# Kernel optimization log

Hardware: AMD Instinct MI355X
Metric: run time of the kernel (lower is better)

## Reference

```python
import jax, jax.numpy as jnp
import numpy as np

NUM_NODES = 4
WEIGHT = 2
IN_C = 128
OUT_C = 128
N = 128
T = 512
BN_EPS = 1e-5


def _shift_index(A, node_num, channels, weight):
    """Faithful numpy port of Modified_shift_gcn.shift(). A: binarized [V,V]."""
    idx = np.arange(node_num * channels).reshape(node_num, channels)
    idx_copy = idx.copy()
    for i in range(node_num):
        current_A = A[i].copy()
        current_A[i] = 0
        neighbors = np.nonzero(current_A)[0]
        j = 0
        counter_i = i + 1
        while j < channels:
            next_node = counter_i % node_num
            if j < weight:
                j += weight
            elif next_node == i:
                j += weight
                counter_i += 1
            elif next_node in neighbors:
                idx[i][j:j + weight] = idx_copy[next_node][j:j + weight]
                j += weight
                counter_i += 1
            else:
                idx[i][j] = idx_copy[next_node][j]
                j += 1
                counter_i += 1
    return idx.flatten()


def setup_inputs() -> dict:
    key = jax.random.key(0)
    k1, k2 = jax.random.split(key)
    # A summed over num_subset then binarized, as in __init__
    adj = np.array([[0, 1, 0, 1], [1, 0, 1, 0], [0, 1, 0, 1], [1, 0, 1, 0]], dtype=np.float64)
    A = np.stack([adj, adj, adj]).sum(0)
    A = (A != 0).astype(np.float64)
    shift_in = jnp.asarray(_shift_index(A.copy(), NUM_NODES, IN_C, WEIGHT), dtype=jnp.int32)
    shift_out = jnp.asarray(_shift_index(A.copy(), NUM_NODES, OUT_C, WEIGHT), dtype=jnp.int32)
    x = jax.random.normal(k1, (N, IN_C, T, NUM_NODES), dtype=jnp.float32)
    Linear_weight = jax.random.normal(k2, (IN_C, OUT_C), dtype=jnp.float32) * float(np.sqrt(1.0 / OUT_C))
    Linear_bias = jnp.zeros((1, 1, OUT_C), dtype=jnp.float32)
    Feature_Mask = jnp.zeros((1, NUM_NODES, IN_C), dtype=jnp.float32)
    bn_gamma = jnp.ones((NUM_NODES * OUT_C,), dtype=jnp.float32)
    bn_beta = jnp.zeros((NUM_NODES * OUT_C,), dtype=jnp.float32)
    return {"x": x, "Linear_weight": Linear_weight, "Linear_bias": Linear_bias,
            "Feature_Mask": Feature_Mask, "bn_gamma": bn_gamma, "bn_beta": bn_beta,
            "shift_in": shift_in, "shift_out": shift_out}


def reference(x, Linear_weight, Linear_bias, Feature_Mask, bn_gamma, bn_beta, shift_in, shift_out):
    n, c, t, v = x.shape
    d = Linear_weight.shape[1]
    # [N,C,T,V] -> [N*T, V*C]
    h = jnp.transpose(x, (0, 2, 3, 1)).reshape(n * t, v * c)
    # shift-in gather
    h = jnp.take(h, shift_in, axis=1)
    # feature mask (tanh + 1) and pointwise linear over channels
    h = h.reshape(n * t, v, c) * (jnp.tanh(Feature_Mask) + 1.0)
    h = jnp.einsum('nvc,cd->nvd', h, Linear_weight) + Linear_bias
    # shift-out gather
    h = h.reshape(n * t, v * d)
    h = jnp.take(h, shift_out, axis=1)
    # BatchNorm1d over the N*T batch dim (training-mode batch stats, biased var)
    mean = jnp.mean(h, axis=0)
    var = jnp.mean(jnp.square(h - mean), axis=0)
    h = (h - mean) * jax.lax.rsqrt(var + BN_EPS) * bn_gamma + bn_beta
    # back to [N,C_out,T,V], residual (down is identity since in==out), ReLU
    out = jnp.transpose(h.reshape(n, t, v, d), (0, 3, 1, 2))
    return jax.nn.relu(out + x)
```

## Files before the change

### kernel.cpp

```cpp
#include <hip/hip_runtime.h>

typedef __attribute__((ext_vector_type(4))) float f32x4;
typedef __attribute__((ext_vector_type(8))) short s16x8;

#define DEV __device__ __forceinline__

namespace {
constexpr int CH = 128;
constexpr int TDIM = 512;
constexpr int NBLK = 512;
constexpr float INV_ROWS = 1.0f / 65536.0f;
constexpr float EPS = 1e-5f;

DEV unsigned short f2bf(float f) {
  unsigned int u = __float_as_uint(f);
  u = (u + 0x7FFFu + ((u >> 16) & 1u)) >> 16;
  return (unsigned short)u;
}

DEV unsigned int pack2bf(float lo, float hi) {
  unsigned int ua = __float_as_uint(lo) + 0x8000u;
  unsigned int ub = __float_as_uint(hi) + 0x8000u;
#if __has_builtin(__builtin_amdgcn_perm)
  return __builtin_amdgcn_perm(ub, ua, 0x07060302u);
#else
  return (ub & 0xFFFF0000u) | (ua >> 16);
#endif
}

DEV void lds_barrier() {
  asm volatile("s_waitcnt lgkmcnt(0)" ::: "memory");
  __builtin_amdgcn_s_barrier();
  asm volatile("" ::: "memory");
}

DEV float maskval(float x) { return 2.0f / (1.0f + __expf(-2.0f * x)); }

DEV int xgi(int b, int v, int t, int c) {
  return (((b << 2) + v) * 16 + t) * 128 + (c ^ ((t & 7) << 3));
}
}

template <int PHASE>
__global__ __launch_bounds__(512) void gcn_fused(
    const float* __restrict__ x, const float* __restrict__ W,
    const float* __restrict__ FM, const int* __restrict__ shin,
    const int* __restrict__ shout, const float* __restrict__ tab,
    float* __restrict__ part, float* __restrict__ out) {
  __shared__ __align__(16) unsigned short xg[2 * 4 * 16 * 128];

  const int tid = threadIdx.x;
  const int lane = tid & 63;
  const int w = tid >> 6;
  const int g4 = lane >> 4;
  const int l16 = lane & 15;
  const int dbase = w * 16;

  const int bid = blockIdx.x;
  const int n = bid >> 2;
  const int tb = (bid & 3) * 128;

  const int tlow = tid & 7;
  const int c0 = (tid >> 3) * 2;

  float mk[2][4];
  unsigned int svp = 0;
#pragma unroll
  for (int i = 0; i < 2; ++i)
#pragma unroll
    for (int v = 0; v < 4; ++v) {
      int j = v * CH + (c0 + i);
      mk[i][v] = maskval(FM[j]);
      svp |= (unsigned int)((shin[j] >> 7) & 3) << ((i * 4 + v) * 2);
    }

  s16x8 wt[4];
#pragma unroll
  for (int kk = 0; kk < 4; ++kk) {
    s16x8 f;
#pragma unroll
    for (int e = 0; e < 8; ++e)
      f[e] = (short)f2bf(W[(kk * 32 + g4 * 8 + e) * CH + dbase + l16]);
    wt[kk] = f;
  }

  unsigned int svo = 0;
  if (PHASE == 2) {
#pragma unroll
    for (int r = 0; r < 4; ++r) {
      int d = dbase + g4 * 4 + r;
#pragma unroll
      for (int v = 0; v < 4; ++v)
        svo |= (unsigned int)((shout[v * CH + d] >> 7) & 3) << (r * 8 + v * 2);
    }
  }

  float s2[4][4];
  f32x4 rs[2];
  if (PHASE == 1) {
#pragma unroll
    for (int vo = 0; vo < 4; ++vo)
#pragma unroll
      for (int r = 0; r < 4; ++r) s2[vo][r] = 0.f;
    rs[0] = f32x4{0.f, 0.f, 0.f, 0.f};
    rs[1] = f32x4{0.f, 0.f, 0.f, 0.f};
  }

  const f32x4* xf4 = (const f32x4*)x;
  const float2* tab2 = (const float2*)tab;

  f32x4 pa[2][2], pb[2][2];
  f32x4 res[2][4];

#define LOADT(SLOT, TILE)                                                 \
  {                                                                       \
    _Pragma("unroll") for (int h = 0; h < 2; ++h) {                       \
      const int tgl = tb + (TILE) * 16 + h * 8 + tlow;                    \
      pa[SLOT][h] = xf4[(n * CH + c0) * TDIM + tgl];                      \
      pb[SLOT][h] = xf4[(n * CH + c0 + 1) * TDIM + tgl];                  \
    }                                                                     \
  }

#define RESLOAD(SLOT, TILE)                                               \
  {                                                                       \
    const int tgr = tb + (TILE) * 16 + l16;                               \
    _Pragma("unroll") for (int r = 0; r < 4; ++r) res[SLOT][r] =          \
        xf4[(n * CH + dbase + g4 * 4 + r) * TDIM + tgr];                  \
  }

#define STAGE(BUF, SLOT)                                                  \
  {                                                                       \
    _Pragma("unroll") for (int h = 0; h < 2; ++h) {                       \
      const int t = h * 8 + tlow;                                         \
      if (PHASE == 1) {                                                   \
        rs[0] += pa[SLOT][h];                                             \
        rs[1] += pb[SLOT][h];                                             \
      }                                                                   \
      _Pragma("unroll") for (int v = 0; v < 4; ++v) {                     \
        int s0 = (svp >> ((0 * 4 + v) * 2)) & 3;                          \
        float a = pa[SLOT][h][0];                                         \
        a = (s0 == 1) ? pa[SLOT][h][1] : a;                               \
        a = (s0 == 2) ? pa[SLOT][h][2] : a;                               \
        a = (s0 == 3) ? pa[SLOT][h][3] : a;                               \
        a *= mk[0][v];                                                    \
        int s1 = (svp >> ((1 * 4 + v) * 2)) & 3;                          \
        float b = pb[SLOT][h][0];                                         \
        b = (s1 == 1) ? pb[SLOT][h][1] : b;                               \
        b = (s1 == 2) ? pb[SLOT][h][2] : b;                               \
        b = (s1 == 3) ? pb[SLOT][h][3] : b;                               \
        b *= mk[1][v];                                                    \
        *(unsigned int*)&xg[xgi(BUF, v, t, c0)] = pack2bf(a, b);          \
      }                                                                   \
    }                                                                     \
  }

  {
    LOADT(0, 0)
    LOADT(1, 1)
    if (PHASE == 2) RESLOAD(0, 0)
    STAGE(0, 0)
  }

#pragma unroll
  for (int tile = 0; tile < 8; ++tile) {
    const int buf = tile & 1;
    lds_barrier();

    if (tile < 6) LOADT(buf, tile + 2)
    if (PHASE == 2 && tile < 7) RESLOAD(buf ^ 1, tile + 1)

    f32x4 acc[4];
    const f32x4 z4 = {0.f, 0.f, 0.f, 0.f};
#pragma unroll
    for (int vo = 0; vo < 4; ++vo) acc[vo] = z4;
#pragma unroll
    for (int vo = 0; vo < 4; ++vo) {
      s16x8 bfr[4];
#pragma unroll
      for (int kk = 0; kk < 4; ++kk)
        bfr[kk] = *(const s16x8*)&xg[xgi(buf, vo, l16, kk * 32 + g4 * 8)];
#pragma unroll
      for (int kk = 0; kk < 4; ++kk)
        acc[vo] = __builtin_amdgcn_mfma_f32_16x16x32_bf16(wt[kk], bfr[kk], acc[vo], 0, 0, 0);
    }

    if (PHASE == 1) {
#pragma unroll
      for (int vo = 0; vo < 4; ++vo)
#pragma unroll
        for (int r = 0; r < 4; ++r) s2[vo][r] = fmaf(acc[vo][r], acc[vo][r], s2[vo][r]);
    } else {
      const int tg = tb + tile * 16 + l16;
#pragma unroll
      for (int r = 0; r < 4; ++r) {
        const int d = dbase + g4 * 4 + r;
        f32x4 o;
#pragma unroll
        for (int v = 0; v < 4; ++v) {
          int sv = (svo >> (r * 8 + v * 2)) & 3;
          float ov = acc[0][r];
          ov = (sv == 1) ? acc[1][r] : ov;
          ov = (sv == 2) ? acc[2][r] : ov;
          ov = (sv == 3) ? acc[3][r] : ov;
          float2 ssv = tab2[v * CH + d];
          float y = fmaf(ov, ssv.x, ssv.y) + res[buf][r][v];
          o[v] = fmaxf(y, 0.f);
        }
        *(f32x4*)&out[((n * CH + d) * TDIM + tg) * 4] = o;
      }
    }

    if (tile < 7) STAGE(buf ^ 1, buf ^ 1)
  }
#undef STAGE
#undef RESLOAD
#undef LOADT

  if (PHASE == 1) {
#pragma unroll
    for (int vo = 0; vo < 4; ++vo)
#pragma unroll
      for (int r = 0; r < 4; ++r) {
        float v = s2[vo][r];
        v += __shfl_xor(v, 1, 64);
        v += __shfl_xor(v, 2, 64);
        v += __shfl_xor(v, 4, 64);
        v += __shfl_xor(v, 8, 64);
        if (l16 == 0) part[(vo * CH + dbase + g4 * 4 + r) * NBLK + bid] = v;
      }
#pragma unroll
    for (int i = 0; i < 2; ++i)
#pragma unroll
      for (int v = 0; v < 4; ++v) {
        float vv = rs[i][v];
        vv += __shfl_xor(vv, 1, 64);
        vv += __shfl_xor(vv, 2, 64);
        vv += __shfl_xor(vv, 4, 64);
        if (tlow == 0) part[(512 + (c0 + i) * 4 + v) * NBLK + bid] = vv;
      }
  }
}

__global__ __launch_bounds__(256) void gcn_reduce(const float* __restrict__ part,
                                                  float* __restrict__ sums) {
  __shared__ float acc4[4];
  const int r = blockIdx.x;
  const int t = threadIdx.x;
  const float* row = part + r * NBLK;
  float s = row[t] + row[t + 256];
#pragma unroll
  for (int off = 1; off < 64; off <<= 1) s += __shfl_xor(s, off, 64);
  if ((t & 63) == 0) acc4[t >> 6] = s;
  __syncthreads();
  if (t == 0) sums[r] = acc4[0] + acc4[1] + acc4[2] + acc4[3];
}

__global__ void gcn_finalize(const float* __restrict__ sums,
                             const float* __restrict__ W,
                             const float* __restrict__ FM,
                             const int* __restrict__ shin,
                             const int* __restrict__ shout,
                             const float* __restrict__ gamma,
                             const float* __restrict__ beta,
                             float* __restrict__ tab) {
  __shared__ float q[512];
  __shared__ float meanS[512];
  __shared__ float rstdS[512];
  const int j = threadIdx.x;
  const int vo = j >> 7;
  const int c = j & 127;
  const int sv = (shin[j] >> 7) & 3;
  q[j] = maskval(FM[j]) * sums[512 + c * 4 + sv];
  __syncthreads();
  const int d = c;
  float acc = 0.f;
#pragma unroll 8
  for (int cc = 0; cc < 128; ++cc) acc = fmaf(W[cc * CH + d], q[vo * CH + cc], acc);
  const float mean = acc * INV_ROWS;
  const float var = sums[j] * INV_ROWS - mean * mean;
  meanS[j] = mean;
  rstdS[j] = rsqrtf(var + EPS);
  __syncthreads();
  const int so = shout[j];
  const float sc = rstdS[so] * gamma[j];
  const float sh = beta[j] - meanS[so] * sc;
  tab[2 * j] = sc;
  tab[2 * j + 1] = sh;
}

extern "C" void kernel_launch(void* const* d_in, const int* in_sizes, int n_in,
                              void* d_out, int out_size, void* d_ws, size_t ws_size,
                              hipStream_t stream) {
  const float* x = (const float*)d_in[0];
  const float* W = (const float*)d_in[1];
  const float* FM = (const float*)d_in[3];
  const float* gamma = (const float*)d_in[4];
  const float* beta = (const float*)d_in[5];
  const int* shin = (const int*)d_in[6];
  const int* shout = (const int*)d_in[7];
  float* out = (float*)d_out;

  float* part = (float*)d_ws;
  float* sums = part + 1024 * NBLK;
  float* tab = sums + 1024;

  gcn_fused<1><<<dim3(NBLK), dim3(512), 0, stream>>>(x, W, FM, shin, shout, tab, part, out);
  gcn_reduce<<<dim3(1024), dim3(256), 0, stream>>>(part, sums);
  gcn_finalize<<<dim3(1), dim3(512), 0, stream>>>(sums, W, FM, shin, shout, gamma, beta, tab);
  gcn_fused<2><<<dim3(NBLK), dim3(512), 0, stream>>>(x, W, FM, shin, shout, tab, part, out);
}
```

Before: 111.5 us.

## Split output channels across two blocks with 256-thread workgroups

Each (batch, time-chunk) unit is now processed by two 256-thread blocks, each computing half of the output channels, while still staging all input channels into shared memory. Each thread loads four input channels per tile, and prefetch depth is reduced to one tile, with residual loads issued in-loop rather than prefetched. This is meant to raise block count and occupancy, but it duplicates global reads of the input tile across the two halves and shortens latency hiding.

```diff
diff --git a/kernel.cpp b/kernel.cpp
--- a/kernel.cpp
+++ b/kernel.cpp
@@ -8,7 +8,7 @@
 namespace {
 constexpr int CH = 128;
 constexpr int TDIM = 512;
-constexpr int NBLK = 512;
+constexpr int NUNIT = 512;
 constexpr float INV_ROWS = 1.0f / 65536.0f;
 constexpr float EPS = 1e-5f;
 
@@ -42,7 +42,7 @@
 }
 
 template <int PHASE>
-__global__ __launch_bounds__(512) void gcn_fused(
+__global__ __launch_bounds__(256) void gcn_fused(
     const float* __restrict__ x, const float* __restrict__ W,
     const float* __restrict__ FM, const int* __restrict__ shin,
     const int* __restrict__ shout, const float* __restrict__ tab,
@@ -54,19 +54,20 @@
   const int w = tid >> 6;
   const int g4 = lane >> 4;
   const int l16 = lane & 15;
-  const int dbase = w * 16;
-
   const int bid = blockIdx.x;
-  const int n = bid >> 2;
-  const int tb = (bid & 3) * 128;
+  const int dhalf = bid >> 9;
+  const int unit = bid & 511;
+  const int n = unit >> 2;
+  const int tb = (unit & 3) * 128;
+  const int dbase = dhalf * 64 + w * 16;
 
   const int tlow = tid & 7;
-  const int c0 = (tid >> 3) * 2;
-
-  float mk[2][4];
+  const int c0 = (tid >> 3) * 4;
+
+  float mk[4][4];
   unsigned int svp = 0;
 #pragma unroll
-  for (int i = 0; i < 2; ++i)
+  for (int i = 0; i < 4; ++i)
 #pragma unroll
     for (int v = 0; v < 4; ++v) {
       int j = v * CH + (c0 + i);
@@ -96,69 +97,58 @@
   }
 
   float s2[4][4];
-  f32x4 rs[2];
+  f32x4 rs[4];
   if (PHASE == 1) {
 #pragma unroll
     for (int vo = 0; vo < 4; ++vo)
 #pragma unroll
       for (int r = 0; r < 4; ++r) s2[vo][r] = 0.f;
-    rs[0] = f32x4{0.f, 0.f, 0.f, 0.f};
-    rs[1] = f32x4{0.f, 0.f, 0.f, 0.f};
+#pragma unroll
+    for (int i = 0; i < 4; ++i) rs[i] = f32x4{0.f, 0.f, 0.f, 0.f};
   }
 
   const f32x4* xf4 = (const f32x4*)x;
   const float2* tab2 = (const float2*)tab;
 
-  f32x4 pa[2][2], pb[2][2];
-  f32x4 res[2][4];
-
-#define LOADT(SLOT, TILE)                                                 \
+  f32x4 px[2][4];
+
+#define LOADT(TILE)                                                       \
   {                                                                       \
     _Pragma("unroll") for (int h = 0; h < 2; ++h) {                       \
       const int tgl = tb + (TILE) * 16 + h * 8 + tlow;                    \
-      pa[SLOT][h] = xf4[(n * CH + c0) * TDIM + tgl];                      \
-      pb[SLOT][h] = xf4[(n * CH + c0 + 1) * TDIM + tgl];                  \
+      _Pragma("unroll") for (int i = 0; i < 4; ++i)                       \
+          px[h][i] = xf4[(n * CH + c0 + i) * TDIM + tgl];                 \
     }                                                                     \
   }
 
-#define RESLOAD(SLOT, TILE)                                               \
-  {                                                                       \
-    const int tgr = tb + (TILE) * 16 + l16;                               \
-    _Pragma("unroll") for (int r = 0; r < 4; ++r) res[SLOT][r] =          \
-        xf4[(n * CH + dbase + g4 * 4 + r) * TDIM + tgr];                  \
-  }
-
-#define STAGE(BUF, SLOT)                                                  \
+#define STAGE(BUF)                                                        \
   {                                                                       \
     _Pragma("unroll") for (int h = 0; h < 2; ++h) {                       \
       const int t = h * 8 + tlow;                                         \
       if (PHASE == 1) {                                                   \
-        rs[0] += pa[SLOT][h];                                             \
-        rs[1] += pb[SLOT][h];                                             \
+        _Pragma("unroll") for (int i = 0; i < 4; ++i) rs[i] += px[h][i];  \
       }                                                                   \
       _Pragma("unroll") for (int v = 0; v < 4; ++v) {                     \
-        int s0 = (svp >> ((0 * 4 + v) * 2)) & 3;                          \
-        float a = pa[SLOT][h][0];                                         \
-        a = (s0 == 1) ? pa[SLOT][h][1] : a;                               \
-        a = (s0 == 2) ? pa[SLOT][h][2] : a;                               \
-        a = (s0 == 3) ? pa[SLOT][h][3] : a;                               \
-        a *= mk[0][v];                                                    \
-        int s1 = (svp >> ((1 * 4 + v) * 2)) & 3;                          \
-        float b = pb[SLOT][h][0];                                         \
-        b = (s1 == 1) ? pb[SLOT][h][1] : b;                               \
-        b = (s1 == 2) ? pb[SLOT][h][2] : b;                               \
-        b = (s1 == 3) ? pb[SLOT][h][3] : b;                               \
-        b *= mk[1][v];                                                    \
-        *(unsigned int*)&xg[xgi(BUF, v, t, c0)] = pack2bf(a, b);          \
+        float f[4];                                                       \
+        _Pragma("unroll") for (int i = 0; i < 4; ++i) {                   \
+          int s = (svp >> ((i * 4 + v) * 2)) & 3;                         \
+          float a = px[h][i][0];                                          \
+          a = (s == 1) ? px[h][i][1] : a;                                 \
+          a = (s == 2) ? px[h][i][2] : a;                                 \
+          a = (s == 3) ? px[h][i][3] : a;                                 \
+          f[i] = a * mk[i][v];                                            \
+        }                                                                 \
+        uint2 u;                                                          \
+        u.x = pack2bf(f[0], f[1]);                                        \
+        u.y = pack2bf(f[2], f[3]);                                        \
+        *(uint2*)&xg[xgi(BUF, v, t, c0)] = u;                             \
       }                                                                   \
     }                                                                     \
   }
 
   {
-    LOADT(0, 0)
-    LOADT(1, 1)
-    if (PHASE == 2) RESLOAD(0, 0)
-    STAGE(0, 0)
+    LOADT(0)
+    STAGE(0)
   }
 
 #pragma unroll
@@ -166,8 +156,14 @@
     const int buf = tile & 1;
     lds_barrier();
 
-    if (tile < 6) LOADT(buf, tile + 2)
-    if (PHASE == 2 && tile < 7) RESLOAD(buf ^ 1, tile + 1)
+    if (tile < 7) LOADT(tile + 1)
+
+    const int tg = tb + tile * 16 + l16;
+    f32x4 res[4];
+    if (PHASE == 2) {
+#pragma unroll
+      for (int r = 0; r < 4; ++r) res[r] = xf4[(n * CH + dbase + g4 * 4 + r) * TDIM + tg];
+    }
 
     f32x4 acc[4];
     const f32x4 z4 = {0.f, 0.f, 0.f, 0.f};
@@ -190,7 +186,6 @@
 #pragma unroll
         for (int r = 0; r < 4; ++r) s2[vo][r] = fmaf(acc[vo][r], acc[vo][r], s2[vo][r]);
     } else {
-      const int tg = tb + tile * 16 + l16;
 #pragma unroll
       for (int r = 0; r < 4; ++r) {
         const int d = dbase + g4 * 4 + r;
@@ -203,17 +198,16 @@
           ov = (sv == 2) ? acc[2][r] : ov;
           ov = (sv == 3) ? acc[3][r] : ov;
           float2 ssv = tab2[v * CH + d];
-          float y = fmaf(ov, ssv.x, ssv.y) + res[buf][r][v];
+          float y = fmaf(ov, ssv.x, ssv.y) + res[r][v];
           o[v] = fmaxf(y, 0.f);
         }
         *(f32x4*)&out[((n * CH + d) * TDIM + tg) * 4] = o;
       }
     }
 
-    if (tile < 7) STAGE(buf ^ 1, buf ^ 1)
+    if (tile < 7) STAGE(buf ^ 1)
   }
 #undef STAGE
-#undef RESLOAD
 #undef LOADT
 
   if (PHASE == 1) {
@@ -226,18 +220,20 @@
         v += __shfl_xor(v, 2, 64);
         v += __shfl_xor(v, 4, 64);
         v += __shfl_xor(v, 8, 64);
-        if (l16 == 0) part[(vo * CH + dbase + g4 * 4 + r) * NBLK + bid] = v;
+        if (l16 == 0) part[(vo * CH + dbase + g4 * 4 + r) * NUNIT + unit] = v;
       }
-#pragma unroll
-    for (int i = 0; i < 2; ++i)
-#pragma unroll
-      for (int v = 0; v < 4; ++v) {
-        float vv = rs[i][v];
-        vv += __shfl_xor(vv, 1, 64);
-        vv += __shfl_xor(vv, 2, 64);
-        vv += __shfl_xor(vv, 4, 64);
-        if (tlow == 0) part[(512 + (c0 + i) * 4 + v) * NBLK + bid] = vv;
-      }
+    if (dhalf == 0) {
+#pragma unroll
+      for (int i = 0; i < 4; ++i)
+#pragma unroll
+        for (int v = 0; v < 4; ++v) {
+          float vv = rs[i][v];
+          vv += __shfl_xor(vv, 1, 64);
+          vv += __shfl_xor(vv, 2, 64);
+          vv += __shfl_xor(vv, 4, 64);
+          if (tlow == 0) part[(512 + (c0 + i) * 4 + v) * NUNIT + unit] = vv;
+        }
+    }
   }
 }
 
@@ -246,7 +242,7 @@
   __shared__ float acc4[4];
   const int r = blockIdx.x;
   const int t = threadIdx.x;
-  const float* row = part + r * NBLK;
+  const float* row = part + r * NUNIT;
   float s = row[t] + row[t + 256];
 #pragma unroll
   for (int off = 1; off < 64; off <<= 1) s += __shfl_xor(s, off, 64);
@@ -301,11 +297,11 @@
   float* out = (float*)d_out;
 
   float* part = (float*)d_ws;
-  float* sums = part + 1024 * NBLK;
+  float* sums = part + 1024 * NUNIT;
   float* tab = sums + 1024;
 
-  gcn_fused<1><<<dim3(NBLK), dim3(512), 0, stream>>>(x, W, FM, shin, shout, tab, part, out);
+  gcn_fused<1><<<dim3(2 * NUNIT), dim3(256), 0, stream>>>(x, W, FM, shin, shout, tab, part, out);
   gcn_reduce<<<dim3(1024), dim3(256), 0, stream>>>(part, sums);
   gcn_finalize<<<dim3(1), dim3(512), 0, stream>>>(sums, W, FM, shin, shout, gamma, beta, tab);
-  gcn_fused<2><<<dim3(NBLK), dim3(512), 0, stream>>>(x, W, FM, shin, shout, tab, part, out);
-}
+  gcn_fused<2><<<dim3(2 * NUNIT), dim3(256), 0, stream>>>(x, W, FM, shin, shout, tab, part, out);
+}
```

Result: slower. 163.0 us (+46.2%).
